# Kernel optimization log

Measured on AMD Instinct MI355X. Metric: run time of the kernel, lower is better.

## Reference

```python
import jax, jax.numpy as jnp
import numpy as np

HIDDEN = 128
NUM_LAYERS = 3
N_NODES = 100000
N_EDGES = 400000
NUM_GRAPHS = 2048


def setup_inputs() -> dict:
    key = jax.random.key(0)
    ks = jax.random.split(key, 10)
    x = jax.random.normal(ks[0], (N_NODES, 1), dtype=jnp.float32)
    edge_index = jax.random.randint(ks[1], (2, N_EDGES), 0, N_NODES, dtype=jnp.int64)
    batch = jnp.sort(jax.random.randint(ks[2], (N_NODES,), 0, NUM_GRAPHS, dtype=jnp.int64))
    s = 1.0 / np.sqrt(HIDDEN)
    W_in = jax.random.normal(ks[3], (1, HIDDEN), dtype=jnp.float32) * s
    b_in = jnp.zeros((HIDDEN,), dtype=jnp.float32)
    W_convs = jax.random.normal(ks[4], (NUM_LAYERS, HIDDEN, HIDDEN), dtype=jnp.float32) * s
    b_convs = jnp.zeros((NUM_LAYERS, HIDDEN), dtype=jnp.float32)
    W_out = jax.random.normal(ks[5], (HIDDEN, HIDDEN), dtype=jnp.float32) * s
    b_out = jnp.zeros((HIDDEN,), dtype=jnp.float32)
    return {"x": x, "edge_index": edge_index, "batch": batch, "num_graphs": NUM_GRAPHS,
            "W_in": W_in, "b_in": b_in, "W_convs": W_convs, "b_convs": b_convs,
            "W_out": W_out, "b_out": b_out}


def reference(x, edge_index, batch, num_graphs, W_in, b_in, W_convs, b_convs, W_out, b_out):
    n_nodes = x.shape[0]
    src, dst = edge_index[0], edge_index[1]
    # GCN symmetric normalization with self-loops: deg = in-degree + 1
    deg = jax.ops.segment_sum(jnp.ones_like(dst, dtype=x.dtype), dst, num_segments=n_nodes) + 1.0
    dinv = deg ** -0.5  # [N]
    edge_norm = (dinv[src] * dinv[dst])[:, None]  # [E,1]
    self_norm = (dinv * dinv)[:, None]            # [N,1], self-loop weight

    h = jax.nn.relu(x @ W_in + b_in)  # [N,H]
    for l in range(W_convs.shape[0]):
        hw = h @ W_convs[l]  # [N,H]
        agg = jax.ops.segment_sum(edge_norm * hw[src], dst, num_segments=n_nodes)
        h = jax.nn.relu(agg + self_norm * hw + b_convs[l])
        # dropout is identity in eval mode

    # global mean pool over graphs
    sums = jax.ops.segment_sum(h, batch, num_segments=num_graphs)  # [G,H]
    cnt = jax.ops.segment_sum(jnp.ones((n_nodes,), dtype=h.dtype), batch, num_segments=num_graphs)
    g = sums / jnp.maximum(cnt, 1.0)[:, None]
    return jax.nn.relu(g @ W_out + b_out)
```

## Files before the change

### kernel.cpp

```cpp
#include <hip/hip_runtime.h>

#define HID 128

typedef __attribute__((ext_vector_type(8))) short short8;
typedef __attribute__((ext_vector_type(4))) float floatx4;

__device__ __forceinline__ float bflo(unsigned u){ return __uint_as_float(u << 16); }
__device__ __forceinline__ float bfhi(unsigned u){ return __uint_as_float(u & 0xffff0000u); }
__device__ __forceinline__ unsigned packbf2(float a, float b){
  unsigned ua = __float_as_uint(a), ub = __float_as_uint(b);
  ua = (ua + 0x7fffu + ((ua >> 16) & 1u)) >> 16;
  ub = (ub + 0x7fffu + ((ub >> 16) & 1u)) >> 16;
  return (ua & 0xffffu) | ((ub & 0xffffu) << 16);
}
__device__ __forceinline__ short8 as_s8(uint4 v){ short8 r; __builtin_memcpy(&r, &v, 16); return r; }

__global__ __launch_bounds__(256) void k_init(int* __restrict__ cnt, int N,
                                              int2* __restrict__ ew, int E,
                                              const float* __restrict__ Wc, uint4* __restrict__ wf,
                                              int zb){
  if ((int)blockIdx.x < zb) {
    int i = blockIdx.x*256 + threadIdx.x;
    int n4 = N >> 2;
    if (i < n4) ((int4*)cnt)[i] = (int4){0,0,0,0};
    if (blockIdx.x == 0 && threadIdx.x == 0) {
      for (int r = n4*4; r < N; ++r) cnt[r] = 0;
      for (int r = 0; r < 4; ++r) { int2 z; z.x = 0; z.y = 0; ew[E + r] = z; }
    }
    return;
  }
  int t = ((int)blockIdx.x - zb)*256 + threadIdx.x;
  if (t >= 3*2048) return;
  int l = t >> 11, r = t & 2047;
  int kt = r >> 9, ct = (r >> 6) & 7, lane = r & 63;
  int kbase = kt*32 + (lane >> 4)*8;
  int m = ct*16 + (lane & 15);
  const float* Wl = Wc + l*16384;
  float v[8];
  #pragma unroll
  for (int i = 0; i < 8; ++i) v[i] = Wl[(kbase + i)*128 + m];
  uint4 o;
  o.x = packbf2(v[0], v[1]);
  o.y = packbf2(v[2], v[3]);
  o.z = packbf2(v[4], v[5]);
  o.w = packbf2(v[6], v[7]);
  wf[t] = o;
}

__global__ __launch_bounds__(256) void k_deg(const int* __restrict__ dst, int* __restrict__ cnt, int E){
  int e = blockIdx.x*256 + threadIdx.x;
  if (e < E) atomicAdd(&cnt[dst[e]], 1);
}

__global__ __launch_bounds__(1024) void k_scan1(const int* __restrict__ cnt, int* __restrict__ rp,
                                                int* __restrict__ bsum, float* __restrict__ dinv, int N){
  __shared__ int s[1024];
  int t = threadIdx.x;
  int i = blockIdx.x*1024 + t;
  int v = (i < N) ? cnt[i] : 0;
  s[t] = v;
  __syncthreads();
  for (int d = 1; d < 1024; d <<= 1) {
    int add = (t >= d) ? s[t - d] : 0;
    __syncthreads();
    s[t] += add;
    __syncthreads();
  }
  if (i < N) {
    rp[i] = s[t] - v;
    dinv[i] = 1.0f / sqrtf((float)v + 1.0f);
  }
  if (t == 1023) bsum[blockIdx.x] = s[1023];
}

__global__ __launch_bounds__(1024) void k_scan3(int* __restrict__ rp, int* __restrict__ cursor,
                                                const int* __restrict__ bsum, int nb, int N){
  __shared__ int s[128];
  int t = threadIdx.x;
  if (t < 128) s[t] = (t < nb) ? bsum[t] : 0;
  __syncthreads();
  for (int d = 1; d < 128; d <<= 1) {
    int add = 0;
    if (t < 128 && t >= d) add = s[t - d];
    __syncthreads();
    if (t < 128) s[t] += add;
    __syncthreads();
  }
  int base = (blockIdx.x > 0) ? s[blockIdx.x - 1] : 0;
  int i = blockIdx.x*1024 + t;
  if (i < N) {
    int v = rp[i] + base;
    rp[i] = v;
    cursor[i] = v;
  }
  if (blockIdx.x == 0 && t == 0) rp[N] = s[nb - 1];
}

__global__ __launch_bounds__(256) void k_fill_gemm0(const int* __restrict__ src, const int* __restrict__ dst,
                                                    int* __restrict__ cursor, int2* __restrict__ ew,
                                                    const float* __restrict__ dinv, int E, int fb,
                                                    const float* __restrict__ x,
                                                    const float* __restrict__ Win,
                                                    const float* __restrict__ bin,
                                                    const uint4* __restrict__ wf,
                                                    unsigned short* __restrict__ hwout, int N){
  __shared__ uint4 lwf[2048];
  __shared__ float sw[128], sb[128];
  if ((int)blockIdx.x < fb) {
    int e = blockIdx.x*256 + threadIdx.x;
    if (e < E){
      int d = dst[e], s = src[e];
      int pos = atomicAdd(&cursor[d], 1);
      int2 pk; pk.x = s; pk.y = __float_as_int(dinv[s]);
      ew[pos] = pk;
    }
    return;
  }
  int t = threadIdx.x;
  #pragma unroll
  for (int j = 0; j < 8; ++j) lwf[t + j*256] = wf[t + j*256];
  if (t < 128) { sw[t] = Win[t]; sb[t] = bin[t]; }
  __syncthreads();
  int lane = t & 63, w = t >> 6;
  int rb = ((int)blockIdx.x - fb)*128 + w*32;
  int nrow0 = rb + (lane & 15);
  int nrow1 = nrow0 + 16;
  float xv0 = x[nrow0 < N ? nrow0 : N - 1];
  float xv1 = x[nrow1 < N ? nrow1 : N - 1];
  floatx4 acc0[8], acc1[8];
  #pragma unroll
  for (int c = 0; c < 8; ++c) { acc0[c] = (floatx4){0.f,0.f,0.f,0.f}; acc1[c] = (floatx4){0.f,0.f,0.f,0.f}; }
  #pragma unroll
  for (int kt = 0; kt < 4; ++kt) {
    int k0 = kt*32 + (lane >> 4)*8;
    float hv0[8], hv1[8];
    #pragma unroll
    for (int i = 0; i < 8; ++i) {
      float wv = sw[k0 + i], bv = sb[k0 + i];
      hv0[i] = fmaxf(fmaf(xv0, wv, bv), 0.f);
      hv1[i] = fmaxf(fmaf(xv1, wv, bv), 0.f);
    }
    uint4 p0, p1;
    p0.x = packbf2(hv0[0], hv0[1]); p0.y = packbf2(hv0[2], hv0[3]);
    p0.z = packbf2(hv0[4], hv0[5]); p0.w = packbf2(hv0[6], hv0[7]);
    p1.x = packbf2(hv1[0], hv1[1]); p1.y = packbf2(hv1[2], hv1[3]);
    p1.z = packbf2(hv1[4], hv1[5]); p1.w = packbf2(hv1[6], hv1[7]);
    short8 hf0 = as_s8(p0), hf1 = as_s8(p1);
    #pragma unroll
    for (int c = 0; c < 8; ++c) {
      short8 af = as_s8(lwf[(kt*8 + c)*64 + lane]);
      acc0[c] = __builtin_amdgcn_mfma_f32_16x16x32_bf16(af, hf0, acc0[c], 0, 0, 0);
      acc1[c] = __builtin_amdgcn_mfma_f32_16x16x32_bf16(af, hf1, acc1[c], 0, 0, 0);
    }
  }
  if (nrow0 < N) {
    unsigned short* op = hwout + (size_t)nrow0*128 + (lane >> 4)*4;
    #pragma unroll
    for (int c = 0; c < 8; ++c) {
      uint2 pk;
      pk.x = packbf2(acc0[c][0], acc0[c][1]);
      pk.y = packbf2(acc0[c][2], acc0[c][3]);
      *(uint2*)(op + c*16) = pk;
    }
  }
  if (nrow1 < N) {
    unsigned short* op = hwout + (size_t)nrow1*128 + (lane >> 4)*4;
    #pragma unroll
    for (int c = 0; c < 8; ++c) {
      uint2 pk;
      pk.x = packbf2(acc1[c][0], acc1[c][1]);
      pk.y = packbf2(acc1[c][2], acc1[c][3]);
      *(uint2*)(op + c*16) = pk;
    }
  }
}

__global__ __launch_bounds__(256) void k_gemm(const unsigned short* __restrict__ hin,
                                              const uint4* __restrict__ wf,
                                              unsigned short* __restrict__ hwout, int N){
  __shared__ uint4 lwf[2048];
  int t = threadIdx.x;
  #pragma unroll
  for (int j = 0; j < 8; ++j) lwf[t + j*256] = wf[t + j*256];
  __syncthreads();
  int lane = t & 63, w = t >> 6;
  int rb = blockIdx.x*128 + w*32;
  int nrow0 = rb + (lane & 15);
  int nrow1 = nrow0 + 16;
  int nc0 = nrow0 < N ? nrow0 : N - 1;
  int nc1 = nrow1 < N ? nrow1 : N - 1;
  const uint4* hp0 = (const uint4*)(hin + (size_t)nc0*128 + (lane >> 4)*8);
  const uint4* hp1 = (const uint4*)(hin + (size_t)nc1*128 + (lane >> 4)*8);
  floatx4 acc0[8], acc1[8];
  #pragma unroll
  for (int c = 0; c < 8; ++c) { acc0[c] = (floatx4){0.f,0.f,0.f,0.f}; acc1[c] = (floatx4){0.f,0.f,0.f,0.f}; }
  #pragma unroll
  for (int kt = 0; kt < 4; ++kt) {
    short8 hf0 = as_s8(hp0[kt*4]);
    short8 hf1 = as_s8(hp1[kt*4]);
    #pragma unroll
    for (int c = 0; c < 8; ++c) {
      short8 af = as_s8(lwf[(kt*8 + c)*64 + lane]);
      acc0[c] = __builtin_amdgcn_mfma_f32_16x16x32_bf16(af, hf0, acc0[c], 0, 0, 0);
      acc1[c] = __builtin_amdgcn_mfma_f32_16x16x32_bf16(af, hf1, acc1[c], 0, 0, 0);
    }
  }
  if (nrow0 < N) {
    unsigned short* op = hwout + (size_t)nrow0*128 + (lane >> 4)*4;
    #pragma unroll
    for (int c = 0; c < 8; ++c) {
      uint2 pk;
      pk.x = packbf2(acc0[c][0], acc0[c][1]);
      pk.y = packbf2(acc0[c][2], acc0[c][3]);
      *(uint2*)(op + c*16) = pk;
    }
  }
  if (nrow1 < N) {
    unsigned short* op = hwout + (size_t)nrow1*128 + (lane >> 4)*4;
    #pragma unroll
    for (int c = 0; c < 8; ++c) {
      uint2 pk;
      pk.x = packbf2(acc1[c][0], acc1[c][1]);
      pk.y = packbf2(acc1[c][2], acc1[c][3]);
      *(uint2*)(op + c*16) = pk;
    }
  }
}

__global__ __launch_bounds__(256) void k_agg(const uint2* __restrict__ hw2, uint2* __restrict__ h2,
                                             const int* __restrict__ rp, const int2* __restrict__ ew,
                                             const float* __restrict__ dinv,
                                             const float* __restrict__ bias, int N){
  int node = (blockIdx.x * blockDim.x + threadIdx.x) >> 5;
  int c = threadIdx.x & 31;
  if (node >= N) return;
  float dn = dinv[node];
  size_t rbase = (size_t)node * 32;
  uint2 su = hw2[rbase + c];
  float a0 = dn * bflo(su.x), a1 = dn * bfhi(su.x);
  float a2 = dn * bflo(su.y), a3 = dn * bfhi(su.y);
  int e0 = rp[node], e1 = rp[node + 1];
  for (int e = e0; e < e1; e += 4) {
    int2 p0 = ew[e], p1 = ew[e+1], p2 = ew[e+2], p3 = ew[e+3];
    uint2 v0 = hw2[(size_t)p0.x * 32 + c];
    uint2 v1 = hw2[(size_t)p1.x * 32 + c];
    uint2 v2 = hw2[(size_t)p2.x * 32 + c];
    uint2 v3 = hw2[(size_t)p3.x * 32 + c];
    float w0 = __int_as_float(p0.y);
    float w1 = (e + 1 < e1) ? __int_as_float(p1.y) : 0.f;
    float w2 = (e + 2 < e1) ? __int_as_float(p2.y) : 0.f;
    float w3 = (e + 3 < e1) ? __int_as_float(p3.y) : 0.f;
    a0 = fmaf(w0, bflo(v0.x), a0); a1 = fmaf(w0, bfhi(v0.x), a1);
    a2 = fmaf(w0, bflo(v0.y), a2); a3 = fmaf(w0, bfhi(v0.y), a3);
    a0 = fmaf(w1, bflo(v1.x), a0); a1 = fmaf(w1, bfhi(v1.x), a1);
    a2 = fmaf(w1, bflo(v1.y), a2); a3 = fmaf(w1, bfhi(v1.y), a3);
    a0 = fmaf(w2, bflo(v2.x), a0); a1 = fmaf(w2, bfhi(v2.x), a1);
    a2 = fmaf(w2, bflo(v2.y), a2); a3 = fmaf(w2, bfhi(v2.y), a3);
    a0 = fmaf(w3, bflo(v3.x), a0); a1 = fmaf(w3, bfhi(v3.x), a1);
    a2 = fmaf(w3, bflo(v3.y), a2); a3 = fmaf(w3, bfhi(v3.y), a3);
  }
  float4 bv = *(const float4*)(bias + c*4);
  float r0 = fmaxf(fmaf(dn, a0, bv.x), 0.f);
  float r1 = fmaxf(fmaf(dn, a1, bv.y), 0.f);
  float r2 = fmaxf(fmaf(dn, a2, bv.z), 0.f);
  float r3 = fmaxf(fmaf(dn, a3, bv.w), 0.f);
  uint2 o;
  o.x = packbf2(r0, r1);
  o.y = packbf2(r2, r3);
  h2[rbase + c] = o;
}

__global__ __launch_bounds__(256) void k_poolout(const uint4* __restrict__ h4, const int* __restrict__ batch,
                                                 const float* __restrict__ Wout, const float* __restrict__ bout,
                                                 float* __restrict__ out, int N, int G){
  __shared__ float sg[4][128];
  int wv = threadIdx.x >> 6;
  int g = blockIdx.x * 4 + wv;
  int lane = threadIdx.x & 63;
  if (g < G) {
    int lo, hi;
    { int a = 0, b = N; while (a < b) { int m = (a + b) >> 1; if (batch[m] < g) a = m + 1; else b = m; } lo = a; }
    { int a = lo, b = N; while (a < b) { int m = (a + b) >> 1; if (batch[m] < g + 1) a = m + 1; else b = m; } hi = a; }
    int r = lane >> 4;
    int c = lane & 15;
    float a0=0.f,a1=0.f,a2=0.f,a3=0.f,a4=0.f,a5=0.f,a6=0.f,a7=0.f;
    for (int n = lo + r; n < hi; n += 4) {
      uint4 v = h4[(size_t)n*16 + c];
      a0 += bflo(v.x); a1 += bfhi(v.x);
      a2 += bflo(v.y); a3 += bfhi(v.y);
      a4 += bflo(v.z); a5 += bfhi(v.z);
      a6 += bflo(v.w); a7 += bfhi(v.w);
    }
    #pragma unroll
    for (int m = 16; m <= 32; m <<= 1) {
      a0 += __shfl_xor(a0, m, 64); a1 += __shfl_xor(a1, m, 64);
      a2 += __shfl_xor(a2, m, 64); a3 += __shfl_xor(a3, m, 64);
      a4 += __shfl_xor(a4, m, 64); a5 += __shfl_xor(a5, m, 64);
      a6 += __shfl_xor(a6, m, 64); a7 += __shfl_xor(a7, m, 64);
    }
    if (r == 0) {
      float inv = 1.0f / fmaxf((float)(hi - lo), 1.0f);
      float* o = &sg[wv][c*8];
      o[0] = a0*inv; o[1] = a1*inv; o[2] = a2*inv; o[3] = a3*inv;
      o[4] = a4*inv; o[5] = a5*inv; o[6] = a6*inv; o[7] = a7*inv;
    }
  }
  __syncthreads();
  if (g < G) {
    float acc0 = 0.f, acc1 = 0.f;
    #pragma unroll 4
    for (int k = 0; k < 128; ++k) {
      float hv = sg[wv][k];
      acc0 = fmaf(hv, Wout[k*128 + lane],      acc0);
      acc1 = fmaf(hv, Wout[k*128 + lane + 64], acc1);
    }
    out[(size_t)g*128 + lane]      = fmaxf(acc0 + bout[lane],      0.f);
    out[(size_t)g*128 + lane + 64] = fmaxf(acc1 + bout[lane + 64], 0.f);
  }
}

extern "C" void kernel_launch(void* const* d_in, const int* in_sizes, int n_in,
                              void* d_out, int out_size, void* d_ws, size_t ws_size,
                              hipStream_t stream){
  (void)n_in; (void)ws_size;
  const float* x       = (const float*)d_in[0];
  const int*   ei      = (const int*)d_in[1];
  const int*   batch   = (const int*)d_in[2];
  const float* W_in    = (const float*)d_in[4];
  const float* b_in    = (const float*)d_in[5];
  const float* W_convs = (const float*)d_in[6];
  const float* b_convs = (const float*)d_in[7];
  const float* W_out   = (const float*)d_in[8];
  const float* b_out   = (const float*)d_in[9];
  float* out = (float*)d_out;

  int N = in_sizes[0];
  int E = in_sizes[1] / 2;
  int G = out_size / HID;

  char* p = (char*)d_ws;
  auto alloc = [&](size_t bytes) -> char* {
    char* r = p; p += (bytes + 255) & ~(size_t)255; return r;
  };
  unsigned* h      = (unsigned*)alloc((size_t)N * 64 * 4);
  unsigned* hw     = (unsigned*)alloc((size_t)N * 64 * 4);
  uint4*    wf     = (uint4*)   alloc(3 * 2048 * 16);
  float*    dinv   = (float*)   alloc((size_t)N * 4);
  int*      cnt    = (int*)     alloc((size_t)N * 4);
  int*      rp     = (int*)     alloc((size_t)(N + 1) * 4);
  int*      cursor = (int*)     alloc((size_t)(N + 1) * 4);
  int2*     ew     = (int2*)    alloc((size_t)(E + 4) * 8);
  int*      bsum   = (int*)     alloc(4096);

  const int* src  = ei;
  const int* dstp = ei + E;

  int zb = (N/4 + 255) / 256;
  k_init<<<zb + 24, 256, 0, stream>>>(cnt, N, ew, E, W_convs, wf, zb);
  k_deg <<<(E + 255) / 256, 256, 0, stream>>>(dstp, cnt, E);
  int nb = (N + 1023) / 1024;
  k_scan1<<<nb, 1024, 0, stream>>>(cnt, rp, bsum, dinv, N);
  k_scan3<<<nb, 1024, 0, stream>>>(rp, cursor, bsum, nb, N);

  int fb = (E + 255) / 256;
  int gb = (N + 127) / 128;
  k_fill_gemm0<<<fb + gb, 256, 0, stream>>>(src, dstp, cursor, ew, dinv, E, fb,
                                            x, W_in, b_in, wf, (unsigned short*)hw, N);

  k_agg <<<(N + 7) / 8, 256, 0, stream>>>((const uint2*)hw, (uint2*)h, rp, ew, dinv, b_convs, N);
  for (int l = 1; l < 3; ++l) {
    k_gemm<<<gb, 256, 0, stream>>>((const unsigned short*)h, wf + l * 2048,
                                   (unsigned short*)hw, N);
    k_agg <<<(N + 7) / 8, 256, 0, stream>>>((const uint2*)hw, (uint2*)h, rp, ew, dinv,
                                            b_convs + l * HID, N);
  }

  k_poolout<<<(G + 3) / 4, 256, 0, stream>>>((const uint4*)h, batch, W_out, b_out, out, N, G);
}
```

Measured before the change: 206.8 us.

## Fuse scan into single decoupled-lookback kernel and process two nodes per aggregation group

Replaces the two-pass block scan (scan1 + scan3) with a single-pass decoupled-lookback scan that uses an atomic ticket and per-block state flags, removing one launch and a re-read of rp. The aggregation kernel now has each 32-lane group handle two adjacent nodes, interleaving their edge loops so more independent gathers are in flight and fewer blocks are launched. The edge padding grows to 8 entries. The cost is spin-waiting in the scan and divergence when the two nodes have unequal degrees.

Result: slower. 226.7 us (+9.6%).

```diff
diff --git a/kernel.cpp b/kernel.cpp
--- a/kernel.cpp
+++ b/kernel.cpp
@@ -18,14 +18,20 @@
 __global__ __launch_bounds__(256) void k_init(int* __restrict__ cnt, int N,
                                               int2* __restrict__ ew, int E,
                                               const float* __restrict__ Wc, uint4* __restrict__ wf,
-                                              int zb){
+                                              long long* __restrict__ states, int* __restrict__ ticket,
+                                              int nbk, int zb){
   if ((int)blockIdx.x < zb) {
     int i = blockIdx.x*256 + threadIdx.x;
     int n4 = N >> 2;
     if (i < n4) ((int4*)cnt)[i] = (int4){0,0,0,0};
-    if (blockIdx.x == 0 && threadIdx.x == 0) {
-      for (int r = n4*4; r < N; ++r) cnt[r] = 0;
-      for (int r = 0; r < 4; ++r) { int2 z; z.x = 0; z.y = 0; ew[E + r] = z; }
+    if (blockIdx.x == 0) {
+      int t = threadIdx.x;
+      if (t < nbk) states[t] = 0;
+      if (t == 0) {
+        *ticket = 0;
+        for (int r = n4*4; r < N; ++r) cnt[r] = 0;
+        for (int r = 0; r < 8; ++r) { int2 z; z.x = 0; z.y = 0; ew[E + r] = z; }
+      }
     }
     return;
   }
@@ -52,48 +58,78 @@
   if (e < E) atomicAdd(&cnt[dst[e]], 1);
 }
 
-__global__ __launch_bounds__(1024) void k_scan1(const int* __restrict__ cnt, int* __restrict__ rp,
-                                                int* __restrict__ bsum, float* __restrict__ dinv, int N){
-  __shared__ int s[1024];
+__global__ __launch_bounds__(256) void k_scan(const int* __restrict__ cnt,
+                                              int* __restrict__ rp, int* __restrict__ cursor,
+                                              float* __restrict__ dinv,
+                                              int* __restrict__ ticket, long long* __restrict__ states,
+                                              int N, int nbk){
+  __shared__ int sb;
+  __shared__ int s[256];
+  __shared__ long long sbase;
   int t = threadIdx.x;
-  int i = blockIdx.x*1024 + t;
-  int v = (i < N) ? cnt[i] : 0;
-  s[t] = v;
-  __syncthreads();
-  for (int d = 1; d < 1024; d <<= 1) {
-    int add = (t >= d) ? s[t - d] : 0;
+  if (t == 0) sb = atomicAdd(ticket, 1);
+  __syncthreads();
+  int bid = sb;
+  int base_i = bid*1024 + t*4;
+  int4 v = (int4){0,0,0,0};
+  if (base_i + 3 < N) v = *(const int4*)(cnt + base_i);
+  else if (base_i < N) {
+    v.x = cnt[base_i];
+    if (base_i+1 < N) v.y = cnt[base_i+1];
+    if (base_i+2 < N) v.z = cnt[base_i+2];
+  }
+  int tsum = v.x + v.y + v.z + v.w;
+  s[t] = tsum;
+  __syncthreads();
+  for (int d = 1; d < 256; d <<= 1) {
+    int add = (t >= d) ? s[t-d] : 0;
     __syncthreads();
     s[t] += add;
     __syncthreads();
   }
-  if (i < N) {
-    rp[i] = s[t] - v;
-    dinv[i] = 1.0f / sqrtf((float)v + 1.0f);
-  }
-  if (t == 1023) bsum[blockIdx.x] = s[1023];
-}
-
-__global__ __launch_bounds__(1024) void k_scan3(int* __restrict__ rp, int* __restrict__ cursor,
-                                                const int* __restrict__ bsum, int nb, int N){
-  __shared__ int s[128];
-  int t = threadIdx.x;
-  if (t < 128) s[t] = (t < nb) ? bsum[t] : 0;
-  __syncthreads();
-  for (int d = 1; d < 128; d <<= 1) {
-    int add = 0;
-    if (t < 128 && t >= d) add = s[t - d];
-    __syncthreads();
-    if (t < 128) s[t] += add;
-    __syncthreads();
-  }
-  int base = (blockIdx.x > 0) ? s[blockIdx.x - 1] : 0;
-  int i = blockIdx.x*1024 + t;
-  if (i < N) {
-    int v = rp[i] + base;
-    rp[i] = v;
-    cursor[i] = v;
-  }
-  if (blockIdx.x == 0 && t == 0) rp[N] = s[nb - 1];
+  int excl_t = s[t] - tsum;
+  int blocksum = s[255];
+  if (t == 0) {
+    if (bid == 0) {
+      __hip_atomic_store(&states[0], ((long long)blocksum << 2) | 2,
+                         __ATOMIC_RELEASE, __HIP_MEMORY_SCOPE_AGENT);
+      sbase = 0;
+    } else {
+      __hip_atomic_store(&states[bid], ((long long)blocksum << 2) | 1,
+                         __ATOMIC_RELEASE, __HIP_MEMORY_SCOPE_AGENT);
+      long long excl = 0; int pred = bid - 1;
+      while (true) {
+        long long st = __hip_atomic_load(&states[pred], __ATOMIC_ACQUIRE, __HIP_MEMORY_SCOPE_AGENT);
+        int f = (int)(st & 3);
+        if (f == 0) continue;
+        excl += (st >> 2);
+        if (f == 2) break;
+        --pred;
+      }
+      __hip_atomic_store(&states[bid], ((excl + (long long)blocksum) << 2) | 2,
+                         __ATOMIC_RELEASE, __HIP_MEMORY_SCOPE_AGENT);
+      sbase = excl;
+    }
+  }
+  __syncthreads();
+  int base = (int)sbase;
+  int p0 = base + excl_t;
+  int p1 = p0 + v.x, p2 = p1 + v.y, p3 = p2 + v.z;
+  if (base_i + 3 < N) {
+    *(int4*)(rp + base_i)     = (int4){p0,p1,p2,p3};
+    *(int4*)(cursor + base_i) = (int4){p0,p1,p2,p3};
+    float4 dv;
+    dv.x = 1.0f/sqrtf((float)v.x + 1.0f);
+    dv.y = 1.0f/sqrtf((float)v.y + 1.0f);
+    dv.z = 1.0f/sqrtf((float)v.z + 1.0f);
+    dv.w = 1.0f/sqrtf((float)v.w + 1.0f);
+    *(float4*)(dinv + base_i) = dv;
+  } else if (base_i < N) {
+    rp[base_i] = p0; cursor[base_i] = p0; dinv[base_i] = 1.0f/sqrtf((float)v.x + 1.0f);
+    if (base_i+1 < N){ rp[base_i+1]=p1; cursor[base_i+1]=p1; dinv[base_i+1]=1.0f/sqrtf((float)v.y+1.0f); }
+    if (base_i+2 < N){ rp[base_i+2]=p2; cursor[base_i+2]=p2; dinv[base_i+2]=1.0f/sqrtf((float)v.z+1.0f); }
+  }
+  if (bid == nbk - 1 && t == 255) rp[N] = base + blocksum;
 }
 
 __global__ __launch_bounds__(256) void k_fill_gemm0(const int* __restrict__ src, const int* __restrict__ dst,
@@ -231,43 +267,83 @@
                                              const int* __restrict__ rp, const int2* __restrict__ ew,
                                              const float* __restrict__ dinv,
                                              const float* __restrict__ bias, int N){
-  int node = (blockIdx.x * blockDim.x + threadIdx.x) >> 5;
+  int pairid = (blockIdx.x * blockDim.x + threadIdx.x) >> 5;
   int c = threadIdx.x & 31;
-  if (node >= N) return;
-  float dn = dinv[node];
-  size_t rbase = (size_t)node * 32;
-  uint2 su = hw2[rbase + c];
-  float a0 = dn * bflo(su.x), a1 = dn * bfhi(su.x);
-  float a2 = dn * bflo(su.y), a3 = dn * bfhi(su.y);
-  int e0 = rp[node], e1 = rp[node + 1];
-  for (int e = e0; e < e1; e += 4) {
-    int2 p0 = ew[e], p1 = ew[e+1], p2 = ew[e+2], p3 = ew[e+3];
-    uint2 v0 = hw2[(size_t)p0.x * 32 + c];
-    uint2 v1 = hw2[(size_t)p1.x * 32 + c];
-    uint2 v2 = hw2[(size_t)p2.x * 32 + c];
-    uint2 v3 = hw2[(size_t)p3.x * 32 + c];
-    float w0 = __int_as_float(p0.y);
-    float w1 = (e + 1 < e1) ? __int_as_float(p1.y) : 0.f;
-    float w2 = (e + 2 < e1) ? __int_as_float(p2.y) : 0.f;
-    float w3 = (e + 3 < e1) ? __int_as_float(p3.y) : 0.f;
-    a0 = fmaf(w0, bflo(v0.x), a0); a1 = fmaf(w0, bfhi(v0.x), a1);
-    a2 = fmaf(w0, bflo(v0.y), a2); a3 = fmaf(w0, bfhi(v0.y), a3);
-    a0 = fmaf(w1, bflo(v1.x), a0); a1 = fmaf(w1, bfhi(v1.x), a1);
-    a2 = fmaf(w1, bflo(v1.y), a2); a3 = fmaf(w1, bfhi(v1.y), a3);
-    a0 = fmaf(w2, bflo(v2.x), a0); a1 = fmaf(w2, bfhi(v2.x), a1);
-    a2 = fmaf(w2, bflo(v2.y), a2); a3 = fmaf(w2, bfhi(v2.y), a3);
-    a0 = fmaf(w3, bflo(v3.x), a0); a1 = fmaf(w3, bfhi(v3.x), a1);
-    a2 = fmaf(w3, bflo(v3.y), a2); a3 = fmaf(w3, bfhi(v3.y), a3);
+  int nA = pairid * 2;
+  if (nA >= N) return;
+  int nB = nA + 1;
+  bool hasB = nB < N;
+  float dnA = dinv[nA];
+  float dnB = hasB ? dinv[nB] : 0.f;
+  size_t rbA = (size_t)nA * 32;
+  size_t rbB = (size_t)(hasB ? nB : nA) * 32;
+  uint2 sA = hw2[rbA + c];
+  uint2 sB = hw2[rbB + c];
+  int e0A = rp[nA];
+  int e1A = rp[nA + 1];
+  int e1B = hasB ? rp[nB + 1] : e1A;
+  float a0 = dnA*bflo(sA.x), a1 = dnA*bfhi(sA.x), a2 = dnA*bflo(sA.y), a3 = dnA*bfhi(sA.y);
+  float b0 = dnB*bflo(sB.x), b1 = dnB*bfhi(sB.x), b2 = dnB*bflo(sB.y), b3 = dnB*bfhi(sB.y);
+  int eA = e0A, eB = e1A;
+  while (eA < e1A || eB < e1B) {
+    if (eA < e1A) {
+      int2 p0 = ew[eA], p1 = ew[eA+1], p2 = ew[eA+2], p3 = ew[eA+3];
+      uint2 v0 = hw2[(size_t)p0.x * 32 + c];
+      uint2 v1 = hw2[(size_t)p1.x * 32 + c];
+      uint2 v2 = hw2[(size_t)p2.x * 32 + c];
+      uint2 v3 = hw2[(size_t)p3.x * 32 + c];
+      float w0 = __int_as_float(p0.y);
+      float w1 = (eA + 1 < e1A) ? __int_as_float(p1.y) : 0.f;
+      float w2 = (eA + 2 < e1A) ? __int_as_float(p2.y) : 0.f;
+      float w3 = (eA + 3 < e1A) ? __int_as_float(p3.y) : 0.f;
+      a0 = fmaf(w0, bflo(v0.x), a0); a1 = fmaf(w0, bfhi(v0.x), a1);
+      a2 = fmaf(w0, bflo(v0.y), a2); a3 = fmaf(w0, bfhi(v0.y), a3);
+      a0 = fmaf(w1, bflo(v1.x), a0); a1 = fmaf(w1, bfhi(v1.x), a1);
+      a2 = fmaf(w1, bflo(v1.y), a2); a3 = fmaf(w1, bfhi(v1.y), a3);
+      a0 = fmaf(w2, bflo(v2.x), a0); a1 = fmaf(w2, bfhi(v2.x), a1);
+      a2 = fmaf(w2, bflo(v2.y), a2); a3 = fmaf(w2, bfhi(v2.y), a3);
+      a0 = fmaf(w3, bflo(v3.x), a0); a1 = fmaf(w3, bfhi(v3.x), a1);
+      a2 = fmaf(w3, bflo(v3.y), a2); a3 = fmaf(w3, bfhi(v3.y), a3);
+      eA += 4;
+    }
+    if (eB < e1B) {
+      int2 p0 = ew[eB], p1 = ew[eB+1], p2 = ew[eB+2], p3 = ew[eB+3];
+      uint2 v0 = hw2[(size_t)p0.x * 32 + c];
+      uint2 v1 = hw2[(size_t)p1.x * 32 + c];
+      uint2 v2 = hw2[(size_t)p2.x * 32 + c];
+      uint2 v3 = hw2[(size_t)p3.x * 32 + c];
+      float w0 = __int_as_float(p0.y);
+      float w1 = (eB + 1 < e1B) ? __int_as_float(p1.y) : 0.f;
+      float w2 = (eB + 2 < e1B) ? __int_as_float(p2.y) : 0.f;
+      float w3 = (eB + 3 < e1B) ? __int_as_float(p3.y) : 0.f;
+      b0 = fmaf(w0, bflo(v0.x), b0); b1 = fmaf(w0, bfhi(v0.x), b1);
+      b2 = fmaf(w0, bflo(v0.y), b2); b3 = fmaf(w0, bfhi(v0.y), b3);
+      b0 = fmaf(w1, bflo(v1.x), b0); b1 = fmaf(w1, bfhi(v1.x), b1);
+      b2 = fmaf(w1, bflo(v1.y), b2); b3 = fmaf(w1, bfhi(v1.y), b3);
+      b0 = fmaf(w2, bflo(v2.x), b0); b1 = fmaf(w2, bfhi(v2.x), b1);
+      b2 = fmaf(w2, bflo(v2.y), b2); b3 = fmaf(w2, bfhi(v2.y), b3);
+      b0 = fmaf(w3, bflo(v3.x), b0); b1 = fmaf(w3, bfhi(v3.x), b1);
+      b2 = fmaf(w3, bflo(v3.y), b2); b3 = fmaf(w3, bfhi(v3.y), b3);
+      eB += 4;
+    }
   }
   float4 bv = *(const float4*)(bias + c*4);
-  float r0 = fmaxf(fmaf(dn, a0, bv.x), 0.f);
-  float r1 = fmaxf(fmaf(dn, a1, bv.y), 0.f);
-  float r2 = fmaxf(fmaf(dn, a2, bv.z), 0.f);
-  float r3 = fmaxf(fmaf(dn, a3, bv.w), 0.f);
-  uint2 o;
-  o.x = packbf2(r0, r1);
-  o.y = packbf2(r2, r3);
-  h2[rbase + c] = o;
+  {
+    float r0 = fmaxf(fmaf(dnA, a0, bv.x), 0.f);
+    float r1 = fmaxf(fmaf(dnA, a1, bv.y), 0.f);
+    float r2 = fmaxf(fmaf(dnA, a2, bv.z), 0.f);
+    float r3 = fmaxf(fmaf(dnA, a3, bv.w), 0.f);
+    uint2 o; o.x = packbf2(r0, r1); o.y = packbf2(r2, r3);
+    h2[rbA + c] = o;
+  }
+  if (hasB) {
+    float r0 = fmaxf(fmaf(dnB, b0, bv.x), 0.f);
+    float r1 = fmaxf(fmaf(dnB, b1, bv.y), 0.f);
+    float r2 = fmaxf(fmaf(dnB, b2, bv.z), 0.f);
+    float r3 = fmaxf(fmaf(dnB, b3, bv.w), 0.f);
+    uint2 o; o.x = packbf2(r0, r1); o.y = packbf2(r2, r3);
+    h2[rbB + c] = o;
+  }
 }
 
 __global__ __launch_bounds__(256) void k_poolout(const uint4* __restrict__ h4, const int* __restrict__ batch,
@@ -342,37 +418,38 @@
   auto alloc = [&](size_t bytes) -> char* {
     char* r = p; p += (bytes + 255) & ~(size_t)255; return r;
   };
-  unsigned* h      = (unsigned*)alloc((size_t)N * 64 * 4);
-  unsigned* hw     = (unsigned*)alloc((size_t)N * 64 * 4);
-  uint4*    wf     = (uint4*)   alloc(3 * 2048 * 16);
-  float*    dinv   = (float*)   alloc((size_t)N * 4);
-  int*      cnt    = (int*)     alloc((size_t)N * 4);
-  int*      rp     = (int*)     alloc((size_t)(N + 1) * 4);
-  int*      cursor = (int*)     alloc((size_t)(N + 1) * 4);
-  int2*     ew     = (int2*)    alloc((size_t)(E + 4) * 8);
-  int*      bsum   = (int*)     alloc(4096);
+  unsigned*   h      = (unsigned*)  alloc((size_t)N * 64 * 4);
+  unsigned*   hw     = (unsigned*)  alloc((size_t)N * 64 * 4);
+  uint4*      wf     = (uint4*)     alloc(3 * 2048 * 16);
+  float*      dinv   = (float*)     alloc((size_t)N * 4);
+  int*        cnt    = (int*)       alloc((size_t)N * 4);
+  int*        rp     = (int*)       alloc((size_t)(N + 1) * 4);
+  int*        cursor = (int*)       alloc((size_t)(N + 1) * 4);
+  int2*       ew     = (int2*)      alloc((size_t)(E + 8) * 8);
+  long long*  states = (long long*) alloc(256 * 8);
+  int*        ticket = (int*)       alloc(256);
 
   const int* src  = ei;
   const int* dstp = ei + E;
 
-  int zb = (N/4 + 255) / 256;
-  k_init<<<zb + 24, 256, 0, stream>>>(cnt, N, ew, E, W_convs, wf, zb);
+  int nbk = (N + 1023) / 1024;
+  int zb  = (N/4 + 255) / 256;
+  k_init<<<zb + 24, 256, 0, stream>>>(cnt, N, ew, E, W_convs, wf, states, ticket, nbk, zb);
   k_deg <<<(E + 255) / 256, 256, 0, stream>>>(dstp, cnt, E);
-  int nb = (N + 1023) / 1024;
-  k_scan1<<<nb, 1024, 0, stream>>>(cnt, rp, bsum, dinv, N);
-  k_scan3<<<nb, 1024, 0, stream>>>(rp, cursor, bsum, nb, N);
+  k_scan<<<nbk, 256, 0, stream>>>(cnt, rp, cursor, dinv, ticket, states, N, nbk);
 
   int fb = (E + 255) / 256;
   int gb = (N + 127) / 128;
   k_fill_gemm0<<<fb + gb, 256, 0, stream>>>(src, dstp, cursor, ew, dinv, E, fb,
                                             x, W_in, b_in, wf, (unsigned short*)hw, N);
 
-  k_agg <<<(N + 7) / 8, 256, 0, stream>>>((const uint2*)hw, (uint2*)h, rp, ew, dinv, b_convs, N);
+  int aggb = ((N + 1) / 2 * 32 + 255) / 256;
+  k_agg <<<aggb, 256, 0, stream>>>((const uint2*)hw, (uint2*)h, rp, ew, dinv, b_convs, N);
   for (int l = 1; l < 3; ++l) {
     k_gemm<<<gb, 256, 0, stream>>>((const unsigned short*)h, wf + l * 2048,
                                    (unsigned short*)hw, N);
-    k_agg <<<(N + 7) / 8, 256, 0, stream>>>((const uint2*)hw, (uint2*)h, rp, ew, dinv,
-                                            b_convs + l * HID, N);
+    k_agg <<<aggb, 256, 0, stream>>>((const uint2*)hw, (uint2*)h, rp, ew, dinv,
+                                     b_convs + l * HID, N);
   }
 
   k_poolout<<<(G + 3) / 4, 256, 0, stream>>>((const uint4*)h, batch, W_out, b_out, out, N, G);
```
